# Performance work log

Hardware: AMD Instinct MI355X
Metric: run time of the kernel (lower is better)

Reference implementation:

```python
import jax, jax.numpy as jnp
import numpy as np

N_NODES = 200000
N_EDGES = 6400000
N_GRAPHS = 1000


def setup_inputs() -> dict:
    key = jax.random.key(0)
    ks = jax.random.split(key, 8)
    x = jax.random.normal(ks[0], (N_NODES, 2), dtype=jnp.float32)
    edge_index = jax.random.randint(ks[1], (2, N_EDGES), 0, N_NODES, dtype=jnp.int32)
    batch = jnp.sort(jax.random.randint(ks[2], (N_NODES,), 0, N_GRAPHS, dtype=jnp.int32))
    W1 = jax.random.normal(ks[3], (2, 16), dtype=jnp.float32) * (1.0 / np.sqrt(2))
    b1 = jnp.zeros((16,), jnp.float32)
    W2 = jax.random.normal(ks[4], (16, 32), dtype=jnp.float32) * (1.0 / np.sqrt(16))
    b2 = jnp.zeros((32,), jnp.float32)
    Wfc1 = jax.random.normal(ks[5], (32, 16), dtype=jnp.float32) * (1.0 / np.sqrt(32))
    bfc1 = jnp.zeros((16,), jnp.float32)
    Wfc2 = jax.random.normal(ks[6], (16, 1), dtype=jnp.float32) * (1.0 / np.sqrt(16))
    bfc2 = jnp.zeros((1,), jnp.float32)
    return {"x": x, "edge_index": edge_index, "batch": batch,
            "W1": W1, "b1": b1, "W2": W2, "b2": b2,
            "Wfc1": Wfc1, "bfc1": bfc1, "Wfc2": Wfc2, "bfc2": bfc2}


def _gcn_norm(edge_index, n_nodes):
    # PyG GCNConv default: add self loops, symmetric normalization.
    loops = jnp.arange(n_nodes, dtype=edge_index.dtype)
    src = jnp.concatenate([edge_index[0], loops])  # message source (row)
    dst = jnp.concatenate([edge_index[1], loops])  # aggregation target (col)
    deg = jax.ops.segment_sum(jnp.ones_like(dst, jnp.float32), dst, num_segments=n_nodes)
    dinv = jnp.where(deg > 0, jax.lax.rsqrt(jnp.maximum(deg, 1.0)), 0.0)
    norm = dinv[src] * dinv[dst]  # [E + N]
    return src, dst, norm


def _gcn_conv(h, W, b, src, dst, norm, n_nodes):
    h = h @ W                                      # transform first (small width)
    msg = h[src] * norm[:, None]                   # gather + scale: [E+N, F]
    out = jax.ops.segment_sum(msg, dst, num_segments=n_nodes)
    return out + b


def reference(x, edge_index, batch, W1, b1, W2, b2, Wfc1, bfc1, Wfc2, bfc2):
    n = x.shape[0]
    src, dst, norm = _gcn_norm(edge_index, n)
    h = jax.nn.relu(_gcn_conv(x, W1, b1, src, dst, norm, n))
    h = jax.nn.relu(_gcn_conv(h, W2, b2, src, dst, norm, n))
    # global_mean_pool over graph ids
    sums = jax.ops.segment_sum(h, batch, num_segments=N_GRAPHS)
    cnts = jax.ops.segment_sum(jnp.ones((n,), h.dtype), batch, num_segments=N_GRAPHS)
    pooled = sums / jnp.maximum(cnts, 1.0)[:, None]  # [G, 32]
    out = jax.nn.relu(pooled @ Wfc1 + bfc1)
    out = out @ Wfc2 + bfc2                          # [G, 1]
    return out.squeeze(-1)
```

## Files before the change

kernel.cpp:

```cpp
#include <hip/hip_runtime.h>
#include <hip/hip_fp16.h>

static inline size_t align256(size_t x) { return (x + 255) & ~size_t(255); }

#define CAP 36864

__global__ __launch_bounds__(1024) void k_scatter(const int* __restrict__ ei,
                                                  int* __restrict__ bcursor,
                                                  unsigned* __restrict__ bdata, int E) {
    __shared__ int lcount[256];
    __shared__ int gbase[256];
    int t = threadIdx.x;
    if (t < 256) lcount[t] = 0;
    __syncthreads();
    int chunk = blockIdx.x * 16384;
    int srcv[16], bkt[16], rank[16], dl[16];
#pragma unroll
    for (int k = 0; k < 8; ++k) {
        int e = chunk + k * 2048 + 2 * t;
        int k2 = 2 * k;
        bkt[k2] = -1; bkt[k2 + 1] = -1;
        if (e < E) {
            int2 sp = *(const int2*)(ei + e);
            int2 dp = *(const int2*)(ei + E + e);
            srcv[k2] = sp.x; bkt[k2] = dp.x >> 10; dl[k2] = dp.x & 1023;
            rank[k2] = atomicAdd(&lcount[bkt[k2]], 1);
            srcv[k2 + 1] = sp.y; bkt[k2 + 1] = dp.y >> 10; dl[k2 + 1] = dp.y & 1023;
            rank[k2 + 1] = atomicAdd(&lcount[bkt[k2 + 1]], 1);
        }
    }
    __syncthreads();
    if (t < 256) {
        int c = lcount[t];
        gbase[t] = t * CAP + (c ? atomicAdd(&bcursor[t], c) : 0);
    }
    __syncthreads();
#pragma unroll
    for (int k = 0; k < 16; ++k) {
        if (bkt[k] >= 0)
            bdata[gbase[bkt[k]] + rank[k]] = ((unsigned)dl[k] << 18) | (unsigned)srcv[k];
    }
}

__global__ __launch_bounds__(1024) void k_build(const unsigned* __restrict__ bdata,
                                                const int* __restrict__ bcursor,
                                                int* __restrict__ row_ptr,
                                                float* __restrict__ dinv,
                                                int* __restrict__ col,
                                                const float* __restrict__ x,
                                                float2* __restrict__ xt,
                                                int N, int E, int NBv) {
    __shared__ int curs[1024];
    __shared__ int sums[256];
    __shared__ int bsc[256];
    __shared__ int stage[CAP];
    int* hist = stage;
    int bkt = blockIdx.x;
    int t = threadIdx.x;
    if (t < 256) bsc[t] = (t < NBv) ? bcursor[t] : 0;
    __syncthreads();
    for (int off = 1; off < 256; off <<= 1) {
        int xv = 0;
        if (t < 256 && t >= off) xv = bsc[t - off];
        __syncthreads();
        if (t < 256) bsc[t] += xv;
        __syncthreads();
    }
    int count = bcursor[bkt];
    int tb = bsc[bkt] - count;
    int fs = bkt * CAP;
    int node0 = bkt << 10;
    int nn = N - node0; if (nn > 1024) nn = 1024;
    hist[t] = 0;
    __syncthreads();
    for (int e = t; e < count; e += 1024)
        atomicAdd(&hist[bdata[fs + e] >> 18], 1);
    __syncthreads();
    int v0 = 0, v1 = 0, v2 = 0, v3 = 0, s = 0;
    if (t < 256) {
        int b4 = t * 4;
        v0 = hist[b4]; v1 = hist[b4 + 1]; v2 = hist[b4 + 2]; v3 = hist[b4 + 3];
        s = v0 + v1 + v2 + v3;
        sums[t] = s;
    }
    __syncthreads();
    for (int off = 1; off < 256; off <<= 1) {
        int xv = 0;
        if (t < 256 && t >= off) xv = sums[t - off];
        __syncthreads();
        if (t < 256) sums[t] += xv;
        __syncthreads();
    }
    if (t < 256) {
        int b4 = t * 4;
        int e0 = sums[t] - s;
        int e1 = e0 + v0, e2 = e1 + v1, e3 = e2 + v2;
        curs[b4] = e0; curs[b4 + 1] = e1; curs[b4 + 2] = e2; curs[b4 + 3] = e3;
        if (b4 < nn)     { row_ptr[node0 + b4]     = tb + e0; dinv[node0 + b4]     = rsqrtf((float)v0 + 1.f); }
        if (b4 + 1 < nn) { row_ptr[node0 + b4 + 1] = tb + e1; dinv[node0 + b4 + 1] = rsqrtf((float)v1 + 1.f); }
        if (b4 + 2 < nn) { row_ptr[node0 + b4 + 2] = tb + e2; dinv[node0 + b4 + 2] = rsqrtf((float)v2 + 1.f); }
        if (b4 + 3 < nn) { row_ptr[node0 + b4 + 3] = tb + e3; dinv[node0 + b4 + 3] = rsqrtf((float)v3 + 1.f); }
    }
    if (bkt == NBv - 1 && t == 0) row_ptr[N] = E;
    __syncthreads();
    for (int e = t; e < count; e += 1024) {
        unsigned p = bdata[fs + e];
        int dl = p >> 18;
        int pos = atomicAdd(&curs[dl], 1);
        stage[pos] = (int)(p & 0x3FFFFu);
    }
    __syncthreads();
    for (int i = t; i < count; i += 1024)
        col[tb + i] = stage[i];
    for (int i = t; i < nn; i += 1024) {
        int node = node0 + i;
        float d2 = dinv[node];
        xt[node] = make_float2(x[node * 2] * d2, x[node * 2 + 1] * d2);
    }
}

__global__ __launch_bounds__(256) void k_conv1_fused(const int* __restrict__ rp,
                                                     const int* __restrict__ col,
                                                     const float2* __restrict__ xt,
                                                     const float* __restrict__ dinv,
                                                     const float* __restrict__ W1,
                                                     const float* __restrict__ b1,
                                                     uint2* __restrict__ ht, int n) {
    int gt = blockIdx.x * 256 + threadIdx.x;
    int node = gt >> 2;
    int q = gt & 3;
    if (node >= n) return;
    int rs = rp[node], re = rp[node + 1];
    float a0 = 0.f, a1 = 0.f;
    int e = rs + q;
    for (; e + 28 < re; e += 32) {
        int c[8];
#pragma unroll
        for (int k = 0; k < 8; ++k) c[k] = __builtin_nontemporal_load(col + e + 4 * k);
        float2 v[8];
#pragma unroll
        for (int k = 0; k < 8; ++k) v[k] = xt[c[k]];
#pragma unroll
        for (int k = 0; k < 8; ++k) { a0 += v[k].x; a1 += v[k].y; }
    }
    for (; e + 12 < re; e += 16) {
        int c0 = __builtin_nontemporal_load(col + e);
        int c1 = __builtin_nontemporal_load(col + e + 4);
        int c2 = __builtin_nontemporal_load(col + e + 8);
        int c3 = __builtin_nontemporal_load(col + e + 12);
        float2 v0 = xt[c0];
        float2 v1 = xt[c1];
        float2 v2 = xt[c2];
        float2 v3 = xt[c3];
        a0 += (v0.x + v1.x) + (v2.x + v3.x);
        a1 += (v0.y + v1.y) + (v2.y + v3.y);
    }
    for (; e < re; e += 4) {
        float2 v = xt[__builtin_nontemporal_load(col + e)];
        a0 += v.x; a1 += v.y;
    }
    if (q == 0) { float2 sf = xt[node]; a0 += sf.x; a1 += sf.y; }
    a0 += __shfl_xor(a0, 1); a0 += __shfl_xor(a0, 2);
    a1 += __shfl_xor(a1, 1); a1 += __shfl_xor(a1, 2);
    float dv = dinv[node];
    a0 *= dv; a1 *= dv;
    int f0 = q * 4;
    float v0 = fmaxf(a0 * W1[f0]     + a1 * W1[16 + f0]     + b1[f0],     0.f) * dv;
    float v1 = fmaxf(a0 * W1[f0 + 1] + a1 * W1[16 + f0 + 1] + b1[f0 + 1], 0.f) * dv;
    float v2 = fmaxf(a0 * W1[f0 + 2] + a1 * W1[16 + f0 + 2] + b1[f0 + 2], 0.f) * dv;
    float v3 = fmaxf(a0 * W1[f0 + 3] + a1 * W1[16 + f0 + 3] + b1[f0 + 3], 0.f) * dv;
    __half2 h0 = __floats2half2_rn(v0, v1);
    __half2 h1 = __floats2half2_rn(v2, v3);
    uint2 w;
    w.x = *reinterpret_cast<unsigned*>(&h0);
    w.y = *reinterpret_cast<unsigned*>(&h1);
    ht[(size_t)node * 4 + q] = w;
}

__global__ __launch_bounds__(256) void k_gather2(const int* __restrict__ rp,
                                                 const int* __restrict__ col,
                                                 const __half2* __restrict__ ht,
                                                 const float* __restrict__ dinv,
                                                 float* __restrict__ agg, int N) {
    int gt = blockIdx.x * 256 + threadIdx.x;
    int node = gt >> 3;
    int fq = gt & 7;
    if (node >= N) return;
    int rs = rp[node], re = rp[node + 1];
    const __half2* __restrict__ base = ht + fq;
    float ax = 0.f, ay = 0.f;
    int e = rs;
    for (; e + 16 <= re; e += 16) {
        int c[16];
#pragma unroll
        for (int k = 0; k < 16; ++k) c[k] = __builtin_nontemporal_load(col + e + k);
        float2 v[16];
#pragma unroll
        for (int k = 0; k < 16; ++k) v[k] = __half22float2(base[(size_t)c[k] * 8]);
#pragma unroll
        for (int k = 0; k < 16; ++k) { ax += v[k].x; ay += v[k].y; }
    }
    for (; e + 8 <= re; e += 8) {
        int c[8];
#pragma unroll
        for (int k = 0; k < 8; ++k) c[k] = __builtin_nontemporal_load(col + e + k);
        float2 v[8];
#pragma unroll
        for (int k = 0; k < 8; ++k) v[k] = __half22float2(base[(size_t)c[k] * 8]);
#pragma unroll
        for (int k = 0; k < 8; ++k) { ax += v[k].x; ay += v[k].y; }
    }
    for (; e < re; ++e) {
        float2 v = __half22float2(base[(size_t)col[e] * 8]);
        ax += v.x; ay += v.y;
    }
    {
        float2 v = __half22float2(base[(size_t)node * 8]);
        ax += v.x; ay += v.y;
    }
    float dv = dinv[node];
    __builtin_nontemporal_store(ax * dv, agg + (size_t)node * 16 + 2 * fq);
    __builtin_nontemporal_store(ay * dv, agg + (size_t)node * 16 + 2 * fq + 1);
}

__global__ __launch_bounds__(256) void k_trans_pool(const float* __restrict__ agg,
                                                    const float* __restrict__ W2,
                                                    const float* __restrict__ b2,
                                                    const int* __restrict__ batch,
                                                    float* __restrict__ gsum, int N) {
    __shared__ float aggs[64][17];
    __shared__ float h2s[64][33];
    __shared__ float w2s[512];
    __shared__ float b2s[32];
    __shared__ int   bids[64];
    int t = threadIdx.x;
    if (t < 128) ((float4*)w2s)[t] = ((const float4*)W2)[t];
    if (t < 32)  b2s[t] = b2[t];
    int node0 = blockIdx.x * 64;
    if (t < 64)  bids[t] = (node0 + t < N) ? batch[node0 + t] : -1;
    {
        int nl = t >> 2, q = t & 3;
        int node = node0 + nl;
        float4 v = make_float4(0.f, 0.f, 0.f, 0.f);
        if (node < N) v = *(const float4*)(agg + (size_t)node * 16 + (size_t)q * 4);
        int c0 = q * 4;
        aggs[nl][c0] = v.x; aggs[nl][c0 + 1] = v.y;
        aggs[nl][c0 + 2] = v.z; aggs[nl][c0 + 3] = v.w;
    }
    __syncthreads();
    {
        int nl = t >> 2;
        int jq = (t & 3) * 8;
        float o[8];
#pragma unroll
        for (int j = 0; j < 8; ++j) o[j] = b2s[jq + j];
#pragma unroll
        for (int k = 0; k < 16; ++k) {
            float a = aggs[nl][k];
#pragma unroll
            for (int j = 0; j < 8; ++j) o[j] += a * w2s[k * 32 + jq + j];
        }
#pragma unroll
        for (int j = 0; j < 8; ++j) h2s[nl][jq + j] = fmaxf(o[j], 0.f);
    }
    __syncthreads();
    if (t < 128) {
        int j = t & 31, seg = t >> 5;
        int nbeg = seg * 16, nend = nbeg + 16;
        float acc = 0.f;
        int cur = bids[nbeg];
        for (int n2 = nbeg; n2 < nend; ++n2) {
            int b = bids[n2];
            if (b != cur) {
                if (cur >= 0) atomicAdd(&gsum[(size_t)cur * 32 + j], acc);
                acc = 0.f; cur = b;
            }
            if (b >= 0) acc += h2s[n2][j];
        }
        if (cur >= 0) atomicAdd(&gsum[(size_t)cur * 32 + j], acc);
    }
}

__global__ void k_final(const float* __restrict__ gsum, const int* __restrict__ batch,
                        const float* __restrict__ Wfc1, const float* __restrict__ bfc1,
                        const float* __restrict__ Wfc2, const float* __restrict__ bfc2,
                        float* __restrict__ out, int G, int N) {
    int g = blockIdx.x * blockDim.x + threadIdx.x;
    if (g >= G) return;
    int lo = 0, hi = N;
    while (lo < hi) { int m = (lo + hi) >> 1; if (batch[m] < g) lo = m + 1; else hi = m; }
    int s = lo;
    lo = s; hi = N;
    while (lo < hi) { int m = (lo + hi) >> 1; if (batch[m] < g + 1) lo = m + 1; else hi = m; }
    float cnt = (float)(lo - s);
    float inv = 1.f / fmaxf(cnt, 1.f);
    float p[32];
#pragma unroll
    for (int i = 0; i < 32; ++i) p[i] = gsum[(size_t)g * 32 + i] * inv;
    float o = bfc2[0];
#pragma unroll
    for (int j = 0; j < 16; ++j) {
        float a = bfc1[j];
#pragma unroll
        for (int i = 0; i < 32; ++i) a += p[i] * Wfc1[i * 16 + j];
        o += fmaxf(a, 0.f) * Wfc2[j];
    }
    out[g] = o;
}

extern "C" void kernel_launch(void* const* d_in, const int* in_sizes, int n_in,
                              void* d_out, int out_size, void* d_ws, size_t ws_size,
                              hipStream_t stream) {
    const float* x     = (const float*)d_in[0];
    const int*   ei    = (const int*)d_in[1];
    const int*   batch = (const int*)d_in[2];
    const float* W1    = (const float*)d_in[3];
    const float* b1    = (const float*)d_in[4];
    const float* W2    = (const float*)d_in[5];
    const float* b2    = (const float*)d_in[6];
    const float* Wfc1  = (const float*)d_in[7];
    const float* bfc1  = (const float*)d_in[8];
    const float* Wfc2  = (const float*)d_in[9];
    const float* bfc2  = (const float*)d_in[10];
    float* out = (float*)d_out;

    const int N = in_sizes[0] / 2;
    const int E = in_sizes[1] / 2;
    const int G = out_size;
    const int NBv = (N + 1023) >> 10;

    char* ws = (char*)d_ws;
    size_t off = 0;
    float* dinv    = (float*)(ws + off); off += align256((size_t)N * 4);
    int*   row_ptr = (int*)(ws + off);   off += align256((size_t)(N + 1) * 4);
    int*   bcursor = (int*)(ws + off);   size_t z0 = off; off += align256(256 * 4);
    float* gsum    = (float*)(ws + off); off += align256((size_t)G * 32 * 4);
    size_t zlen = off - z0;
    float2* xt     = (float2*)(ws + off); off += align256((size_t)N * 8);
    __half2* ht    = (__half2*)(ws + off); off += align256((size_t)N * 32);
    float* agg     = (float*)(ws + off); off += align256((size_t)N * 16 * 4);
    int*   col     = (int*)(ws + off);   off += align256((size_t)E * 4);
    unsigned* bdata = (unsigned*)(ws + off); off += align256((size_t)NBv * CAP * 4);

    const int BS = 256;

    hipMemsetAsync(bcursor, 0, zlen, stream);

    k_scatter<<<(E + 16383) / 16384, 1024, 0, stream>>>(ei, bcursor, bdata, E);
    k_build<<<NBv, 1024, 0, stream>>>(bdata, bcursor, row_ptr, dinv, col, x, xt, N, E, NBv);

    k_conv1_fused<<<((size_t)N * 4 + 255) / 256, 256, 0, stream>>>(row_ptr, col, xt, dinv,
                                                                   W1, b1, (uint2*)ht, N);
    k_gather2<<<((size_t)N * 8 + 255) / 256, 256, 0, stream>>>(row_ptr, col, ht, dinv, agg, N);
    k_trans_pool<<<(N + 63) / 64, 256, 0, stream>>>(agg, W2, b2, batch, gsum, N);

    k_final<<<(G + BS - 1) / BS, BS, 0, stream>>>(gsum, batch, Wfc1, bfc1, Wfc2, bfc2,
                                                  out, G, N);
}
```

Before: 244.5 us.

## Split CSR build and fuse first GCN conv into column-staging kernel

The CSR build is split into two kernels. The first computes row_ptr, dinv and the scaled features xt. The second groups the columns in shared memory and then runs the first convolution directly from the staged column indices in LDS, so col no longer has to be re-read from global memory in a separate conv1 kernel. In exchange, each node is now handled by a single thread, which can cause load imbalance on high-degree nodes, and occupancy is limited by the 1024-thread blocks with a large LDS footprint.

After: 227.9 us. 6.8% less time.

```diff
diff --git a/kernel.cpp b/kernel.cpp
--- a/kernel.cpp
+++ b/kernel.cpp
@@ -42,19 +42,16 @@
     }
 }
 
-__global__ __launch_bounds__(1024) void k_build(const unsigned* __restrict__ bdata,
-                                                const int* __restrict__ bcursor,
-                                                int* __restrict__ row_ptr,
-                                                float* __restrict__ dinv,
-                                                int* __restrict__ col,
-                                                const float* __restrict__ x,
-                                                float2* __restrict__ xt,
-                                                int N, int E, int NBv) {
-    __shared__ int curs[1024];
+__global__ __launch_bounds__(1024) void k_build1(const unsigned* __restrict__ bdata,
+                                                 const int* __restrict__ bcursor,
+                                                 int* __restrict__ row_ptr,
+                                                 float* __restrict__ dinv,
+                                                 const float* __restrict__ x,
+                                                 float2* __restrict__ xt,
+                                                 int N, int E, int NBv) {
+    __shared__ int hist[1024];
     __shared__ int sums[256];
     __shared__ int bsc[256];
-    __shared__ int stage[CAP];
-    int* hist = stage;
     int bkt = blockIdx.x;
     int t = threadIdx.x;
     if (t < 256) bsc[t] = (t < NBv) ? bcursor[t] : 0;
@@ -95,13 +92,46 @@
         int b4 = t * 4;
         int e0 = sums[t] - s;
         int e1 = e0 + v0, e2 = e1 + v1, e3 = e2 + v2;
-        curs[b4] = e0; curs[b4 + 1] = e1; curs[b4 + 2] = e2; curs[b4 + 3] = e3;
         if (b4 < nn)     { row_ptr[node0 + b4]     = tb + e0; dinv[node0 + b4]     = rsqrtf((float)v0 + 1.f); }
         if (b4 + 1 < nn) { row_ptr[node0 + b4 + 1] = tb + e1; dinv[node0 + b4 + 1] = rsqrtf((float)v1 + 1.f); }
         if (b4 + 2 < nn) { row_ptr[node0 + b4 + 2] = tb + e2; dinv[node0 + b4 + 2] = rsqrtf((float)v2 + 1.f); }
         if (b4 + 3 < nn) { row_ptr[node0 + b4 + 3] = tb + e3; dinv[node0 + b4 + 3] = rsqrtf((float)v3 + 1.f); }
     }
     if (bkt == NBv - 1 && t == 0) row_ptr[N] = E;
+    __syncthreads();
+    for (int i = t; i < nn; i += 1024) {
+        int node = node0 + i;
+        float d2 = rsqrtf((float)hist[i] + 1.f);
+        xt[node] = make_float2(x[node * 2] * d2, x[node * 2 + 1] * d2);
+    }
+}
+
+__global__ __launch_bounds__(1024) void k_build2(const unsigned* __restrict__ bdata,
+                                                 const int* __restrict__ bcursor,
+                                                 const int* __restrict__ row_ptr,
+                                                 const float2* __restrict__ xt,
+                                                 const float* __restrict__ W1,
+                                                 const float* __restrict__ b1,
+                                                 int* __restrict__ col,
+                                                 uint4* __restrict__ ht,
+                                                 int N, int E, int NBv) {
+    __shared__ int curs[1024];
+    __shared__ int cstart[1024];
+    __shared__ int stage[CAP];
+    __shared__ float w1s[32];
+    __shared__ float b1s[16];
+    int bkt = blockIdx.x;
+    int t = threadIdx.x;
+    if (t < 32) w1s[t] = W1[t];
+    if (t < 16) b1s[t] = b1[t];
+    int count = bcursor[bkt];
+    int fs = bkt * CAP;
+    int node0 = bkt << 10;
+    int nn = N - node0; if (nn > 1024) nn = 1024;
+    int tb = row_ptr[node0];
+    int sl0 = (t < nn) ? (row_ptr[node0 + t] - tb) : 0;
+    curs[t] = sl0;
+    cstart[t] = sl0;
     __syncthreads();
     for (int e = t; e < count; e += 1024) {
         unsigned p = bdata[fs + e];
@@ -112,69 +142,39 @@
     __syncthreads();
     for (int i = t; i < count; i += 1024)
         col[tb + i] = stage[i];
-    for (int i = t; i < nn; i += 1024) {
-        int node = node0 + i;
-        float d2 = dinv[node];
-        xt[node] = make_float2(x[node * 2] * d2, x[node * 2 + 1] * d2);
-    }
-}
-
-__global__ __launch_bounds__(256) void k_conv1_fused(const int* __restrict__ rp,
-                                                     const int* __restrict__ col,
-                                                     const float2* __restrict__ xt,
-                                                     const float* __restrict__ dinv,
-                                                     const float* __restrict__ W1,
-                                                     const float* __restrict__ b1,
-                                                     uint2* __restrict__ ht, int n) {
-    int gt = blockIdx.x * 256 + threadIdx.x;
-    int node = gt >> 2;
-    int q = gt & 3;
-    if (node >= n) return;
-    int rs = rp[node], re = rp[node + 1];
-    float a0 = 0.f, a1 = 0.f;
-    int e = rs + q;
-    for (; e + 28 < re; e += 32) {
-        int c[8];
-#pragma unroll
-        for (int k = 0; k < 8; ++k) c[k] = __builtin_nontemporal_load(col + e + 4 * k);
-        float2 v[8];
-#pragma unroll
-        for (int k = 0; k < 8; ++k) v[k] = xt[c[k]];
-#pragma unroll
-        for (int k = 0; k < 8; ++k) { a0 += v[k].x; a1 += v[k].y; }
-    }
-    for (; e + 12 < re; e += 16) {
-        int c0 = __builtin_nontemporal_load(col + e);
-        int c1 = __builtin_nontemporal_load(col + e + 4);
-        int c2 = __builtin_nontemporal_load(col + e + 8);
-        int c3 = __builtin_nontemporal_load(col + e + 12);
-        float2 v0 = xt[c0];
-        float2 v1 = xt[c1];
-        float2 v2 = xt[c2];
-        float2 v3 = xt[c3];
-        a0 += (v0.x + v1.x) + (v2.x + v3.x);
-        a1 += (v0.y + v1.y) + (v2.y + v3.y);
-    }
-    for (; e < re; e += 4) {
-        float2 v = xt[__builtin_nontemporal_load(col + e)];
-        a0 += v.x; a1 += v.y;
-    }
-    if (q == 0) { float2 sf = xt[node]; a0 += sf.x; a1 += sf.y; }
-    a0 += __shfl_xor(a0, 1); a0 += __shfl_xor(a0, 2);
-    a1 += __shfl_xor(a1, 1); a1 += __shfl_xor(a1, 2);
-    float dv = dinv[node];
-    a0 *= dv; a1 *= dv;
-    int f0 = q * 4;
-    float v0 = fmaxf(a0 * W1[f0]     + a1 * W1[16 + f0]     + b1[f0],     0.f) * dv;
-    float v1 = fmaxf(a0 * W1[f0 + 1] + a1 * W1[16 + f0 + 1] + b1[f0 + 1], 0.f) * dv;
-    float v2 = fmaxf(a0 * W1[f0 + 2] + a1 * W1[16 + f0 + 2] + b1[f0 + 2], 0.f) * dv;
-    float v3 = fmaxf(a0 * W1[f0 + 3] + a1 * W1[16 + f0 + 3] + b1[f0 + 3], 0.f) * dv;
-    __half2 h0 = __floats2half2_rn(v0, v1);
-    __half2 h1 = __floats2half2_rn(v2, v3);
-    uint2 w;
-    w.x = *reinterpret_cast<unsigned*>(&h0);
-    w.y = *reinterpret_cast<unsigned*>(&h1);
-    ht[(size_t)node * 4 + q] = w;
+    if (t < nn) {
+        int node = node0 + t;
+        int sl = cstart[t], el = curs[t];
+        float a0 = 0.f, a1 = 0.f;
+        int e = sl;
+        for (; e + 8 <= el; e += 8) {
+            int c[8];
+#pragma unroll
+            for (int k = 0; k < 8; ++k) c[k] = stage[e + k];
+            float2 v[8];
+#pragma unroll
+            for (int k = 0; k < 8; ++k) v[k] = xt[c[k]];
+#pragma unroll
+            for (int k = 0; k < 8; ++k) { a0 += v[k].x; a1 += v[k].y; }
+        }
+        for (; e < el; ++e) {
+            float2 v = xt[stage[e]];
+            a0 += v.x; a1 += v.y;
+        }
+        float2 sf = xt[node];
+        a0 += sf.x; a1 += sf.y;
+        float dv = rsqrtf((float)(el - sl) + 1.f);
+        a0 *= dv; a1 *= dv;
+        __half2 hv[8];
+#pragma unroll
+        for (int f2 = 0; f2 < 8; ++f2) {
+            float v0 = fmaxf(a0 * w1s[2 * f2]     + a1 * w1s[16 + 2 * f2]     + b1s[2 * f2],     0.f) * dv;
+            float v1 = fmaxf(a0 * w1s[2 * f2 + 1] + a1 * w1s[16 + 2 * f2 + 1] + b1s[2 * f2 + 1], 0.f) * dv;
+            hv[f2] = __floats2half2_rn(v0, v1);
+        }
+        ht[(size_t)node * 2]     = *reinterpret_cast<uint4*>(&hv[0]);
+        ht[(size_t)node * 2 + 1] = *reinterpret_cast<uint4*>(&hv[4]);
+    }
 }
 
 __global__ __launch_bounds__(256) void k_gather2(const int* __restrict__ rp,
@@ -347,11 +347,12 @@
     hipMemsetAsync(bcursor, 0, zlen, stream);
 
     k_scatter<<<(E + 16383) / 16384, 1024, 0, stream>>>(ei, bcursor, bdata, E);
-    k_build<<<NBv, 1024, 0, stream>>>(bdata, bcursor, row_ptr, dinv, col, x, xt, N, E, NBv);
-
-    k_conv1_fused<<<((size_t)N * 4 + 255) / 256, 256, 0, stream>>>(row_ptr, col, xt, dinv,
-                                                                   W1, b1, (uint2*)ht, N);
-    k_gather2<<<((size_t)N * 8 + 255) / 256, 256, 0, stream>>>(row_ptr, col, ht, dinv, agg, N);
+    k_build1<<<NBv, 1024, 0, stream>>>(bdata, bcursor, row_ptr, dinv, x, xt, N, E, NBv);
+    k_build2<<<NBv, 1024, 0, stream>>>(bdata, bcursor, row_ptr, xt, W1, b1, col,
+                                       (uint4*)ht, N, E, NBv);
+
+    k_gather2<<<((size_t)N * 8 + 255) / 256, 256, 0, stream>>>(row_ptr, col, (const __half2*)ht,
+                                                               dinv, agg, N);
     k_trans_pool<<<(N + 63) / 64, 256, 0, stream>>>(agg, W2, b2, batch, gsum, N);
 
     k_final<<<(G + BS - 1) / BS, BS, 0, stream>>>(gsum, batch, Wfc1, bfc1, Wfc2, bfc2,
```
